# Optimization experiments

Measured on AMD Instinct MI355X. Metric: run time of the kernel, lower is better.

Reference implementation:

```python
import jax, jax.numpy as jnp
import numpy as np

N = 100000
E = 1600000
K = 2  # KProp steps


def setup_inputs() -> dict:
    key = jax.random.key(0)
    ks = jax.random.split(key, 8)
    x = jax.random.normal(ks[0], (N, 64), dtype=jnp.float32)
    edge_index = jax.random.randint(ks[1], (2, E), 0, N, dtype=jnp.int32)
    s = 1.0 / np.sqrt(64)
    W2l = jax.random.normal(ks[2], (64, 64), dtype=jnp.float32) * s
    W2r = jax.random.normal(ks[3], (64, 64), dtype=jnp.float32) * s
    b2 = jnp.zeros((64,), dtype=jnp.float32)
    W3l = jax.random.normal(ks[4], (64, 16), dtype=jnp.float32) * s
    W3r = jax.random.normal(ks[5], (64, 16), dtype=jnp.float32) * s
    b3 = jnp.zeros((16,), dtype=jnp.float32)
    return {"x": x, "edge_index": edge_index, "W2l": W2l, "W2r": W2r,
            "b2": b2, "W3l": W3l, "W3r": W3r, "b3": b3}


def reference(x, edge_index, W2l, W2r, b2, W3l, W3r, b3):
    dst, src = edge_index[0], edge_index[1]  # adj_t[i,j]: edge j -> i
    ones = jnp.ones((E,), dtype=x.dtype)
    deg = jax.ops.segment_sum(ones, dst, num_segments=N)  # in-degree
    dinv = jnp.where(deg > 0, jax.lax.rsqrt(jnp.maximum(deg, 1.0)), 0.0)
    w = dinv[dst] * dinv[src]  # gcn_norm weights (no self-loops in norm)

    # KProp: K steps of (D^-1/2 A D^-1/2 + I) @ h  (set_diag adds unit diag)
    h = x
    for _ in range(K):
        h = jax.ops.segment_sum(w[:, None] * h[src], dst, num_segments=N) + h

    degm = jnp.maximum(deg, 1.0)[:, None]

    # SAGEConv 1: mean-neighbor aggregate + root weight
    agg = jax.ops.segment_sum(h[src], dst, num_segments=N) / degm
    h = agg @ W2l + h @ W2r + b2
    h = jax.nn.selu(h)

    # SAGEConv 2
    agg = jax.ops.segment_sum(h[src], dst, num_segments=N) / degm
    h = agg @ W3l + h @ W3r + b3
    return jax.nn.softmax(h, axis=1)
```

## Files before the change

### kernel.cpp

```cpp
#include <hip/hip_runtime.h>
#include <hip/hip_bf16.h>

#define NNODES 100000
#define NEDGES 1600000
#define NBUCK 391
#define BCAP 4800
#define SPLIT_TILE 4096
#define NSPLIT ((NEDGES + SPLIT_TILE - 1) / SPLIT_TILE)
#define NTILES (NNODES / 16)

typedef short short8 __attribute__((ext_vector_type(8)));
typedef unsigned short ushx8 __attribute__((ext_vector_type(8)));
typedef float floatx4 __attribute__((ext_vector_type(4)));

__device__ __forceinline__ unsigned short f2b(float f) {
    unsigned u = __float_as_uint(f);
    u += 0x7fffu + ((u >> 16) & 1u);
    return (unsigned short)(u >> 16);
}

__device__ __forceinline__ void acc8(float* a, ushx8 u) {
#pragma unroll
    for (int i = 0; i < 8; ++i)
        a[i] += __uint_as_float((unsigned)u[i] << 16);
}

__device__ __forceinline__ void acc8s(float* a, ushx8 u, float s) {
#pragma unroll
    for (int i = 0; i < 8; ++i)
        a[i] = fmaf(s, __uint_as_float((unsigned)u[i] << 16), a[i]);
}

__global__ __launch_bounds__(256) void split_kernel(
    const int* __restrict__ dst, const int* __restrict__ src,
    int* __restrict__ gcur, unsigned* __restrict__ fpairs) {
    __shared__ int lhist[NBUCK];
    __shared__ int lstart[NBUCK];
    int t = threadIdx.x;
    for (int i = t; i < NBUCK; i += 256) lhist[i] = 0;
    __syncthreads();
    int base = blockIdx.x * SPLIT_TILE;
    int n = min(SPLIT_TILE, NEDGES - base);
    for (int i = t; i < n; i += 256) {
        atomicAdd(&lhist[dst[base + i] >> 8], 1);
    }
    __syncthreads();
    for (int i = t; i < NBUCK; i += 256) {
        int c = lhist[i];
        lstart[i] = (c > 0) ? atomicAdd(&gcur[i], c) : 0;
        lhist[i] = 0;
    }
    __syncthreads();
    for (int i = t; i < n; i += 256) {
        int d = dst[base + i];
        int s = src[base + i];
        int k = d >> 8;
        int pos = lstart[k] + atomicAdd(&lhist[k], 1);
        fpairs[(size_t)k * BCAP + pos] = ((unsigned)s << 8) | (unsigned)(d & 255);
    }
}

__global__ __launch_bounds__(256) void finalize_kernel(
    const unsigned* __restrict__ fpairs, const int* __restrict__ gcur2,
    const float* __restrict__ x,
    int* __restrict__ col, int* __restrict__ deg, int* __restrict__ rowoff,
    float* __restrict__ dinv, unsigned short* __restrict__ g0b) {
    __shared__ int ldeg[256];
    __shared__ int lcur[256];
    __shared__ float ldi[256];
    __shared__ int lsc[256];
    __shared__ int bb[NBUCK + 1];
    int k = blockIdx.x;
    int t = threadIdx.x;
    int a2 = (2 * t < NBUCK) ? gcur2[2 * t] : 0;
    int b2v = (2 * t + 1 < NBUCK) ? gcur2[2 * t + 1] : 0;
    int ts = a2 + b2v;
    lsc[t] = ts;
    __syncthreads();
    for (int s = 1; s < 256; s <<= 1) {
        int v = (t >= s) ? lsc[t - s] : 0;
        __syncthreads();
        lsc[t] += v;
        __syncthreads();
    }
    int excl2 = lsc[t] - ts;
    if (2 * t < NBUCK) bb[2 * t] = excl2;
    if (2 * t + 1 < NBUCK) bb[2 * t + 1] = excl2 + a2;
    ldeg[t] = 0;
    __syncthreads();
    int node0 = k << 8;
    int ncount = min(256, NNODES - node0);
    int base = bb[k];
    int count = gcur2[k];
    const unsigned* pb = fpairs + (size_t)k * BCAP;
    for (int i = t; i < count; i += 256) {
        atomicAdd(&ldeg[pb[i] & 255], 1);
    }
    __syncthreads();
    int a = ldeg[t];
    lsc[t] = a;
    __syncthreads();
    for (int s = 1; s < 256; s <<= 1) {
        int v = (t >= s) ? lsc[t - s] : 0;
        __syncthreads();
        lsc[t] += v;
        __syncthreads();
    }
    int excl = lsc[t] - a;
    lcur[t] = base + excl;
    if (t < ncount) {
        int n0 = node0 + t;
        rowoff[n0] = base + excl;
        deg[n0] = a;
        float di = (a > 0) ? rsqrtf((float)a) : 0.0f;
        ldi[t] = di;
        dinv[n0] = di;
    }
    __syncthreads();
    for (int i = t; i < count; i += 256) {
        unsigned p = pb[i];
        int dl = (int)(p & 255u);
        int s = (int)(p >> 8);
        int pos = atomicAdd(&lcur[dl], 1);
        col[pos] = s;
    }
    const float4* x4 = (const float4*)x;
    int f4count = ncount * 16;
    int b4 = node0 * 16;
    for (int j = t; j < f4count; j += 256) {
        float di = ldi[j >> 4];
        float4 v = x4[b4 + j];
        ushort4 u;
        u.x = f2b(di * v.x); u.y = f2b(di * v.y);
        u.z = f2b(di * v.z); u.w = f2b(di * v.w);
        *(ushort4*)(g0b + (size_t)(b4 + j) * 4) = u;
    }
}

template <int MODE>
__global__ __launch_bounds__(256) void gatherw_kernel(
    const unsigned short* __restrict__ vin, const float* __restrict__ hinf,
    const unsigned short* __restrict__ hinb,
    unsigned short* __restrict__ out0,
    const int* __restrict__ rowoff, const int* __restrict__ deg,
    const int* __restrict__ col, const float* __restrict__ dinv) {
    int node = blockIdx.x * 4 + (threadIdx.x >> 6);
    int lane = threadIdx.x & 63;
    int sub = lane & 7;
    int g = lane >> 3;
    int beg = rowoff[node];
    int dg = deg[node];
    int end = beg + dg;
    float af[8] = {0.f, 0.f, 0.f, 0.f, 0.f, 0.f, 0.f, 0.f};
    float bf[8] = {0.f, 0.f, 0.f, 0.f, 0.f, 0.f, 0.f, 0.f};
    int e = beg + g;
    for (; e + 8 < end; e += 16) {
        int c0 = col[e];
        int c1 = col[e + 8];
        ushx8 u0 = *(const ushx8*)(vin + (size_t)c0 * 64 + sub * 8);
        ushx8 u1 = *(const ushx8*)(vin + (size_t)c1 * 64 + sub * 8);
        if (MODE == 1) {
            float d0 = dinv[c0];
            float d1 = dinv[c1];
            acc8s(af, u0, d0);
            acc8s(bf, u1, d1);
        } else {
            acc8(af, u0);
            acc8(bf, u1);
        }
    }
    if (e < end) {
        int c0 = col[e];
        ushx8 u0 = *(const ushx8*)(vin + (size_t)c0 * 64 + sub * 8);
        if (MODE == 1) {
            float d0 = dinv[c0];
            acc8s(af, u0, d0);
        } else {
            acc8(af, u0);
        }
    }
#pragma unroll
    for (int i = 0; i < 8; ++i) {
        float v = af[i] + bf[i];
        v += __shfl_xor(v, 8);
        v += __shfl_xor(v, 16);
        v += __shfl_xor(v, 32);
        af[i] = v;
    }
    if (lane < 8) {
        size_t off = (size_t)node * 64 + lane * 8;
        ushx8 uh;
        if (MODE <= 1) {
            float di = dinv[node];
            float hv[8];
            if (MODE == 0) {
                float4 h0 = *(const float4*)(hinf + off);
                float4 h1 = *(const float4*)(hinf + off + 4);
                hv[0] = h0.x; hv[1] = h0.y; hv[2] = h0.z; hv[3] = h0.w;
                hv[4] = h1.x; hv[5] = h1.y; hv[6] = h1.z; hv[7] = h1.w;
            } else {
                ushx8 u = *(const ushx8*)(hinb + off);
#pragma unroll
                for (int i = 0; i < 8; ++i) hv[i] = __uint_as_float((unsigned)u[i] << 16);
            }
#pragma unroll
            for (int i = 0; i < 8; ++i) uh[i] = f2b(hv[i] + di * af[i]);
        } else {
            float r = 1.0f / (float)(dg > 0 ? dg : 1);
#pragma unroll
            for (int i = 0; i < 8; ++i) uh[i] = f2b(af[i] * r);
        }
        *(ushx8*)(out0 + off) = uh;
    }
}

__global__ __launch_bounds__(256) void dense1_mfma(
    const unsigned short* __restrict__ aggb, const unsigned short* __restrict__ hb,
    unsigned short* __restrict__ h3b,
    const float* __restrict__ W2l, const float* __restrict__ W2r,
    const float* __restrict__ b2) {
    __shared__ unsigned short Wt[64 * 144];
    int t = threadIdx.x;
    for (int idx = t; idx < 128 * 64; idx += 256) {
        int k = idx >> 6, j = idx & 63;
        float v = (k < 64) ? W2l[k * 64 + j] : W2r[(k - 64) * 64 + j];
        Wt[j * 144 + k] = f2b(v);
    }
    __syncthreads();
    int wib = t >> 6, lane = t & 63;
    int tile = blockIdx.x * 4 + wib;
    if (tile >= NTILES) return;
    int node0 = tile * 16;
    int jj = lane & 15, kg = lane >> 4;
    short8 bfrag[4][4];
#pragma unroll
    for (int nt = 0; nt < 4; ++nt)
#pragma unroll
        for (int s = 0; s < 4; ++s)
            bfrag[nt][s] = *(const short8*)&Wt[(nt * 16 + jj) * 144 + s * 32 + kg * 8];
    int arow = node0 + jj;
    const unsigned short* ap = aggb + (size_t)arow * 64 + kg * 8;
    const unsigned short* hp = hb + (size_t)arow * 64 + kg * 8;
    short8 afrag[4];
    afrag[0] = *(const short8*)ap;
    afrag[1] = *(const short8*)(ap + 32);
    afrag[2] = *(const short8*)hp;
    afrag[3] = *(const short8*)(hp + 32);
    const float lam = 1.0507009873554804934193349852946f;
    const float alp = 1.6732632423543772848170429916717f;
#pragma unroll
    for (int nt = 0; nt < 4; ++nt) {
        floatx4 acc = {0.f, 0.f, 0.f, 0.f};
#pragma unroll
        for (int s = 0; s < 4; ++s)
            acc = __builtin_amdgcn_mfma_f32_16x16x32_bf16(afrag[s], bfrag[nt][s], acc, 0, 0, 0);
        float bias = b2[nt * 16 + jj];
#pragma unroll
        for (int r = 0; r < 4; ++r) {
            float v = acc[r] + bias;
            float o = (v > 0.0f) ? lam * v : lam * alp * expm1f(v);
            int node = node0 + kg * 4 + r;
            h3b[(size_t)node * 64 + nt * 16 + jj] = f2b(o);
        }
    }
}

__global__ __launch_bounds__(256) void dense2_mfma(
    const unsigned short* __restrict__ aggb, const unsigned short* __restrict__ hb,
    float* __restrict__ out,
    const float* __restrict__ W3l, const float* __restrict__ W3r,
    const float* __restrict__ b3) {
    __shared__ unsigned short Wt[16 * 144];
    int t = threadIdx.x;
    for (int idx = t; idx < 128 * 16; idx += 256) {
        int k = idx >> 4, j = idx & 15;
        float v = (k < 64) ? W3l[k * 16 + j] : W3r[(k - 64) * 16 + j];
        Wt[j * 144 + k] = f2b(v);
    }
    __syncthreads();
    int wib = t >> 6, lane = t & 63;
    int tile = blockIdx.x * 4 + wib;
    if (tile >= NTILES) return;
    int node0 = tile * 16;
    int jj = lane & 15, kg = lane >> 4;
    short8 bfrag[4];
#pragma unroll
    for (int s = 0; s < 4; ++s)
        bfrag[s] = *(const short8*)&Wt[jj * 144 + s * 32 + kg * 8];
    int arow = node0 + jj;
    const unsigned short* ap = aggb + (size_t)arow * 64 + kg * 8;
    const unsigned short* hp = hb + (size_t)arow * 64 + kg * 8;
    short8 afrag[4];
    afrag[0] = *(const short8*)ap;
    afrag[1] = *(const short8*)(ap + 32);
    afrag[2] = *(const short8*)hp;
    afrag[3] = *(const short8*)(hp + 32);
    floatx4 acc = {0.f, 0.f, 0.f, 0.f};
#pragma unroll
    for (int s = 0; s < 4; ++s)
        acc = __builtin_amdgcn_mfma_f32_16x16x32_bf16(afrag[s], bfrag[s], acc, 0, 0, 0);
    float bias = b3[jj];
#pragma unroll
    for (int r = 0; r < 4; ++r) {
        float v = acc[r] + bias;
        float m = v;
        m = fmaxf(m, __shfl_xor(m, 1));
        m = fmaxf(m, __shfl_xor(m, 2));
        m = fmaxf(m, __shfl_xor(m, 4));
        m = fmaxf(m, __shfl_xor(m, 8));
        float ex = expf(v - m);
        float s2 = ex;
        s2 += __shfl_xor(s2, 1);
        s2 += __shfl_xor(s2, 2);
        s2 += __shfl_xor(s2, 4);
        s2 += __shfl_xor(s2, 8);
        int node = node0 + kg * 4 + r;
        out[(size_t)node * 16 + jj] = ex / s2;
    }
}

extern "C" void kernel_launch(void* const* d_in, const int* in_sizes, int n_in,
                              void* d_out, int out_size, void* d_ws, size_t ws_size,
                              hipStream_t stream) {
    const float* x   = (const float*)d_in[0];
    const int*   ei  = (const int*)d_in[1];
    const float* W2l = (const float*)d_in[2];
    const float* W2r = (const float*)d_in[3];
    const float* b2  = (const float*)d_in[4];
    const float* W3l = (const float*)d_in[5];
    const float* W3r = (const float*)d_in[6];
    const float* b3  = (const float*)d_in[7];
    float* out = (float*)d_out;

    const int* dst = ei;
    const int* src = ei + NEDGES;

    char* ws = (char*)d_ws;
    unsigned short* B0 = (unsigned short*)ws; ws += (size_t)NNODES * 64 * 2;
    unsigned short* B1 = (unsigned short*)ws; ws += (size_t)NNODES * 64 * 2;
    unsigned short* B2 = (unsigned short*)ws; ws += (size_t)NNODES * 64 * 2;
    unsigned* fpairs  = (unsigned*)ws; ws += (size_t)NBUCK * BCAP * 4;
    int*      col     = (int*)ws;      ws += (size_t)NEDGES * 4;
    int*      deg     = (int*)ws;      ws += (size_t)NNODES * 4;
    int*      rowoff  = (int*)ws;      ws += (size_t)NNODES * 4;
    float*    dinv    = (float*)ws;    ws += (size_t)NNODES * 4;
    int*      gcur    = (int*)ws;      ws += NBUCK * 4;

    unsigned short* h1b = B1;
    unsigned short* h2b = B0;
    unsigned short* h3b = B1;

    hipMemsetAsync(gcur, 0, NBUCK * 4, stream);

    split_kernel<<<NSPLIT, 256, 0, stream>>>(dst, src, gcur, fpairs);
    finalize_kernel<<<NBUCK, 256, 0, stream>>>(fpairs, gcur, x,
                                               col, deg, rowoff, dinv, B0);

    int nblk = NNODES / 4;
    int ndense = (NTILES + 3) / 4;
    gatherw_kernel<0><<<nblk, 256, 0, stream>>>(B0, x, nullptr, h1b, rowoff, deg, col, dinv);
    gatherw_kernel<1><<<nblk, 256, 0, stream>>>(h1b, nullptr, h1b, h2b, rowoff, deg, col, dinv);
    gatherw_kernel<2><<<nblk, 256, 0, stream>>>(h2b, nullptr, nullptr, B2, rowoff, deg, col, dinv);
    dense1_mfma<<<ndense, 256, 0, stream>>>(B2, h2b, h3b, W2l, W2r, b2);
    gatherw_kernel<2><<<nblk, 256, 0, stream>>>(h3b, nullptr, nullptr, B2, rowoff, deg, col, dinv);
    dense2_mfma<<<ndense, 256, 0, stream>>>(B2, h3b, out, W3l, W3r, b3);
}
```

Baseline: 324.2 us.

## Stash edges in LDS, split x-scaling into its own kernel, vectorize weight loads

The split kernel caches dst indices in shared memory so the second pass does not reload them from global memory. The finalize kernel stashes its bucket pairs in LDS instead of reading fpairs twice. The dinv-scaled bf16 conversion of x moves into a separate fully parallel kernel, which adds one launch but spreads that work across many blocks instead of 391. The dense kernels load weights as float4 when building the transposed LDS tile.

```diff
diff --git a/kernel.cpp b/kernel.cpp
--- a/kernel.cpp
+++ b/kernel.cpp
@@ -36,13 +36,16 @@
     int* __restrict__ gcur, unsigned* __restrict__ fpairs) {
     __shared__ int lhist[NBUCK];
     __shared__ int lstart[NBUCK];
+    __shared__ int ldst[SPLIT_TILE];
     int t = threadIdx.x;
     for (int i = t; i < NBUCK; i += 256) lhist[i] = 0;
     __syncthreads();
     int base = blockIdx.x * SPLIT_TILE;
     int n = min(SPLIT_TILE, NEDGES - base);
     for (int i = t; i < n; i += 256) {
-        atomicAdd(&lhist[dst[base + i] >> 8], 1);
+        int d = dst[base + i];
+        ldst[i] = d;
+        atomicAdd(&lhist[d >> 8], 1);
     }
     __syncthreads();
     for (int i = t; i < NBUCK; i += 256) {
@@ -52,7 +55,7 @@
     }
     __syncthreads();
     for (int i = t; i < n; i += 256) {
-        int d = dst[base + i];
+        int d = ldst[i];
         int s = src[base + i];
         int k = d >> 8;
         int pos = lstart[k] + atomicAdd(&lhist[k], 1);
@@ -62,12 +65,11 @@
 
 __global__ __launch_bounds__(256) void finalize_kernel(
     const unsigned* __restrict__ fpairs, const int* __restrict__ gcur2,
-    const float* __restrict__ x,
     int* __restrict__ col, int* __restrict__ deg, int* __restrict__ rowoff,
-    float* __restrict__ dinv, unsigned short* __restrict__ g0b) {
+    float* __restrict__ dinv) {
+    __shared__ unsigned stash[BCAP];
     __shared__ int ldeg[256];
     __shared__ int lcur[256];
-    __shared__ float ldi[256];
     __shared__ int lsc[256];
     __shared__ int bb[NBUCK + 1];
     int k = blockIdx.x;
@@ -94,7 +96,9 @@
     int count = gcur2[k];
     const unsigned* pb = fpairs + (size_t)k * BCAP;
     for (int i = t; i < count; i += 256) {
-        atomicAdd(&ldeg[pb[i] & 255], 1);
+        unsigned p = pb[i];
+        stash[i] = p;
+        atomicAdd(&ldeg[p & 255], 1);
     }
     __syncthreads();
     int a = ldeg[t];
@@ -112,28 +116,29 @@
         int n0 = node0 + t;
         rowoff[n0] = base + excl;
         deg[n0] = a;
-        float di = (a > 0) ? rsqrtf((float)a) : 0.0f;
-        ldi[t] = di;
-        dinv[n0] = di;
+        dinv[n0] = (a > 0) ? rsqrtf((float)a) : 0.0f;
     }
     __syncthreads();
     for (int i = t; i < count; i += 256) {
-        unsigned p = pb[i];
+        unsigned p = stash[i];
         int dl = (int)(p & 255u);
         int s = (int)(p >> 8);
         int pos = atomicAdd(&lcur[dl], 1);
         col[pos] = s;
     }
-    const float4* x4 = (const float4*)x;
-    int f4count = ncount * 16;
-    int b4 = node0 * 16;
-    for (int j = t; j < f4count; j += 256) {
-        float di = ldi[j >> 4];
-        float4 v = x4[b4 + j];
+}
+
+__global__ __launch_bounds__(256) void g0_kernel(
+    const float* __restrict__ x, const float* __restrict__ dinv,
+    unsigned short* __restrict__ g0b) {
+    int t = blockIdx.x * 256 + threadIdx.x;
+    if (t < NNODES * 16) {
+        float di = dinv[t >> 4];
+        float4 v = ((const float4*)x)[t];
         ushort4 u;
         u.x = f2b(di * v.x); u.y = f2b(di * v.y);
         u.z = f2b(di * v.z); u.w = f2b(di * v.w);
-        *(ushort4*)(g0b + (size_t)(b4 + j) * 4) = u;
+        ((ushort4*)g0b)[t] = u;
     }
 }
 
@@ -221,10 +226,22 @@
     const float* __restrict__ b2) {
     __shared__ unsigned short Wt[64 * 144];
     int t = threadIdx.x;
-    for (int idx = t; idx < 128 * 64; idx += 256) {
-        int k = idx >> 6, j = idx & 63;
-        float v = (k < 64) ? W2l[k * 64 + j] : W2r[(k - 64) * 64 + j];
-        Wt[j * 144 + k] = f2b(v);
+    for (int idx = t; idx < 2048; idx += 256) {
+        int basef = idx * 4;
+        float4 v;
+        int k, j;
+        if (basef < 4096) {
+            v = ((const float4*)W2l)[idx];
+            k = basef >> 6; j = basef & 63;
+        } else {
+            v = ((const float4*)W2r)[idx - 1024];
+            int bf2 = basef - 4096;
+            k = 64 + (bf2 >> 6); j = bf2 & 63;
+        }
+        Wt[j * 144 + k]       = f2b(v.x);
+        Wt[(j + 1) * 144 + k] = f2b(v.y);
+        Wt[(j + 2) * 144 + k] = f2b(v.z);
+        Wt[(j + 3) * 144 + k] = f2b(v.w);
     }
     __syncthreads();
     int wib = t >> 6, lane = t & 63;
@@ -272,10 +289,22 @@
     const float* __restrict__ b3) {
     __shared__ unsigned short Wt[16 * 144];
     int t = threadIdx.x;
-    for (int idx = t; idx < 128 * 16; idx += 256) {
-        int k = idx >> 4, j = idx & 15;
-        float v = (k < 64) ? W3l[k * 16 + j] : W3r[(k - 64) * 16 + j];
-        Wt[j * 144 + k] = f2b(v);
+    for (int idx = t; idx < 512; idx += 256) {
+        int basef = idx * 4;
+        float4 v;
+        int k, j;
+        if (basef < 1024) {
+            v = ((const float4*)W3l)[idx];
+            k = basef >> 4; j = basef & 15;
+        } else {
+            v = ((const float4*)W3r)[idx - 256];
+            int bf2 = basef - 1024;
+            k = 64 + (bf2 >> 4); j = bf2 & 15;
+        }
+        Wt[j * 144 + k]       = f2b(v.x);
+        Wt[(j + 1) * 144 + k] = f2b(v.y);
+        Wt[(j + 2) * 144 + k] = f2b(v.z);
+        Wt[(j + 3) * 144 + k] = f2b(v.w);
     }
     __syncthreads();
     int wib = t >> 6, lane = t & 63;
@@ -353,8 +382,8 @@
     hipMemsetAsync(gcur, 0, NBUCK * 4, stream);
 
     split_kernel<<<NSPLIT, 256, 0, stream>>>(dst, src, gcur, fpairs);
-    finalize_kernel<<<NBUCK, 256, 0, stream>>>(fpairs, gcur, x,
-                                               col, deg, rowoff, dinv, B0);
+    finalize_kernel<<<NBUCK, 256, 0, stream>>>(fpairs, gcur, col, deg, rowoff, dinv);
+    g0_kernel<<<(NNODES * 16 + 255) / 256, 256, 0, stream>>>(x, dinv, B0);
 
     int nblk = NNODES / 4;
     int ndense = (NTILES + 3) / 4;
```

New measurement: 325.0 us. No clear change (+0.2%).
